# Kernel tuning notes

Measured on AMD Instinct MI355X. Metric: run time of the kernel, lower is better.

## Reference

```python
import jax, jax.numpy as jnp
import numpy as np
from jax import lax

# Module config (matches init_kwargs)
FILTERS = 4
C, D_K, H, W = 4, 3, 128, 128   # kernel_size = [c, d, h, w]
ACT_SIZE = (3, 3, 3)            # activate_size
ACT_STRIDE = (3, 1, 1)          # activate_stride
LEAKY_ALPHA = 0.2               # tf.nn.leaky_relu default
BATCH, DEPTH = 4, 16


def setup_inputs() -> dict:
    key = jax.random.key(0)
    kx, kw, kb = jax.random.split(key, 3)
    x = jax.random.normal(kx, (BATCH, C, DEPTH, H, W), jnp.float32)
    # he_normal on the [filters,1,c,d,h,w] maps (fan_in = c*d*h*w)
    scale = np.float32(np.sqrt(2.0 / (C * D_K * H * W)))
    weight = jax.random.normal(kw, (FILTERS, 1, C, D_K, H, W), jnp.float32) * scale
    bias = jax.random.normal(kb, (FILTERS, 1, C, D_K, H, W), jnp.float32) * scale
    return {"x": x, "weight": weight, "bias": bias}


def _forward(x, weight, bias):
    # x: [B, c, D, h, w]; weight/bias: [F, 1, c, d, h, w]
    B, c, D, h, w = x.shape
    F, d = weight.shape[0], weight.shape[3]
    Dout = D - d + 1  # valid depth windows (try/except skips the out-of-range tails)

    # Sliding depth windows: [B, c, Dout, d, h, w] -> [B, Dout, c, d, h, w]
    idx = jnp.arange(Dout)[:, None] + jnp.arange(d)[None, :]
    xw = jnp.transpose(x[:, :, idx], (0, 2, 1, 3, 4, 5))

    # Per-filter affine on each window (vectorized over F and Dout):
    # a[b,f,i] = x_window[b,i] * weight[f,0] + bias[f,0]  -> [B, F, Dout, c, d, h, w]
    a = xw[:, None] * weight[:, 0][None, :, None] + bias[:, 0][None, :, None]
    a = a.reshape(B * F * Dout, c, d, h, w)

    # Non-trainable 'activate' conv: Conv3D(filters=1, kernel=ones, SAME,
    # channels_first, no bias) followed by leaky_relu(alpha=0.2)
    kern = jnp.ones((1, c) + ACT_SIZE, a.dtype)  # OIDHW
    y = lax.conv_general_dilated(
        a, kern, window_strides=ACT_STRIDE, padding='SAME',
        dimension_numbers=('NCDHW', 'OIDHW', 'NCDHW'))
    y = jax.nn.leaky_relu(y, LEAKY_ALPHA)  # [B*F*Dout, 1, dout, h, w]

    dout = y.shape[2]  # = 1 for d=3, stride 3 (SAME)
    # Concatenation over filters (axis=1) then depth (axis=2)
    return y.reshape(B, F, Dout * dout, h, w)


def reference(x, weight, bias):
    return _forward(x, weight, bias)
```

## Files before the change

### kernel.cpp

```cpp
#include <hip/hip_runtime.h>

#define HH    128
#define WW    128
#define CDIM  4
#define DK    3
#define FDIM  4
#define DEPTH 16
#define DOUT  14
#define NB    4
#define HW    (HH * WW)
#define IB    2
#define NIP   (DOUT / IB)
#define TROWS 4
#define HROWS (TROWS + 2)
#define NTILE (HH / TROWS)

__global__ __launch_bounds__(256) void bsum_kernel(const float* __restrict__ bias,
                                                   float* __restrict__ bsum) {
    int idx = blockIdx.x * 256 + threadIdx.x;
    int f  = idx >> 14;
    int hw = idx & 16383;
    const float* bp = bias + f * (CDIM * DK * HW) + hw;
    float s = 0.f;
#pragma unroll
    for (int c = 0; c < CDIM; ++c)
#pragma unroll
        for (int dd = 0; dd < DK; ++dd)
            s += bp[c * (DK * HW) + dd * HW];
    bsum[idx] = s;
}

__global__ __launch_bounds__(256) void linerconv_main(const float* __restrict__ x,
                                                      const float* __restrict__ wgt,
                                                      const float* __restrict__ bsum,
                                                      float* __restrict__ out) {
    const int blk  = blockIdx.x;
    const int tile = blk & (NTILE - 1);
    const int tmp  = blk >> 5;
    const int ip   = tmp % NIP;
    const int b    = tmp / NIP;
    const int i0   = ip * IB;
    const int h0   = tile * TROWS;

    __shared__ float lds[IB][FDIM][HROWS][WW];

    const int tid = threadIdx.x;

    if (tid < HROWS * 32) {
        const int row = tid >> 5;
        const int q   = tid & 31;
        const int g   = h0 - 1 + row;
        if (g >= 0 && g < HH) {
            const int base_hw = g * WW + q * 4;
            float4 a0[FDIM], a1[FDIM];
#pragma unroll
            for (int f = 0; f < FDIM; ++f) {
                float4 bv = *(const float4*)(bsum + f * HW + base_hw);
                a0[f] = bv;
                a1[f] = bv;
            }
            const float* xb = x + b * (CDIM * DEPTH * HW) + i0 * HW + base_hw;
            const float* wb = wgt + base_hw;
#pragma unroll
            for (int c = 0; c < CDIM; ++c) {
                float4 xp[IB + DK - 1];
#pragma unroll
                for (int j = 0; j < IB + DK - 1; ++j)
                    xp[j] = *(const float4*)(xb + c * (DEPTH * HW) + j * HW);
#pragma unroll
                for (int dd = 0; dd < DK; ++dd) {
#pragma unroll
                    for (int f = 0; f < FDIM; ++f) {
                        float4 wv = *(const float4*)(wb + f * (CDIM * DK * HW)
                                                        + c * (DK * HW) + dd * HW);
                        a0[f].x += xp[dd].x * wv.x;
                        a0[f].y += xp[dd].y * wv.y;
                        a0[f].z += xp[dd].z * wv.z;
                        a0[f].w += xp[dd].w * wv.w;
                        a1[f].x += xp[dd + 1].x * wv.x;
                        a1[f].y += xp[dd + 1].y * wv.y;
                        a1[f].z += xp[dd + 1].z * wv.z;
                        a1[f].w += xp[dd + 1].w * wv.w;
                    }
                }
            }
#pragma unroll
            for (int f = 0; f < FDIM; ++f) {
                *(float4*)&lds[0][f][row][q * 4] = a0[f];
                *(float4*)&lds[1][f][row][q * 4] = a1[f];
            }
        } else {
            float4 z = make_float4(0.f, 0.f, 0.f, 0.f);
#pragma unroll
            for (int f = 0; f < FDIM; ++f) {
                *(float4*)&lds[0][f][row][q * 4] = z;
                *(float4*)&lds[1][f][row][q * 4] = z;
            }
        }
    }
    __syncthreads();

    const int w = tid & 127;
    const int s = tid >> 7;
#pragma unroll
    for (int k = 0; k < 4; ++k) {
        const int i2 = k >> 1;
        const int f  = (k & 1) + s * 2;
        const float* Lb = &lds[i2][f][0][0];
        float rs[HROWS];
#pragma unroll
        for (int g = 0; g < HROWS; ++g) {
            const float* Lr = Lb + g * WW;
            float v = Lr[w];
            if (w > 0)   v += Lr[w - 1];
            if (w < 127) v += Lr[w + 1];
            rs[g] = v;
        }
        float* op = out + ((b * FDIM + f) * DOUT + (i0 + i2)) * HW + h0 * WW + w;
#pragma unroll
        for (int r = 0; r < TROWS; ++r) {
            float sum = rs[r] + rs[r + 1] + rs[r + 2];
            float y = (sum >= 0.f) ? sum : 0.2f * sum;
            __builtin_nontemporal_store(y, op + r * WW);
        }
    }
}

extern "C" void kernel_launch(void* const* d_in, const int* in_sizes, int n_in,
                              void* d_out, int out_size, void* d_ws, size_t ws_size,
                              hipStream_t stream) {
    const float* x    = (const float*)d_in[0];
    const float* wgt  = (const float*)d_in[1];
    const float* bias = (const float*)d_in[2];
    float* out  = (float*)d_out;
    float* bsum = (float*)d_ws;

    bsum_kernel<<<256, 256, 0, stream>>>(bias, bsum);
    linerconv_main<<<NB * NIP * NTILE, 256, 0, stream>>>(x, wgt, bsum, out);
}
```

Baseline: 20.89 us.

## Process four depth windows per block and vectorize the box-filter stage

Each block now computes four output depth windows instead of two, with a two-window tail group, so each x slice and weight load is reused across more windows and fewer blocks re-read overlapping inputs. The second stage now has each thread handle four adjacent columns with float4 LDS reads and float4 nontemporal stores, replacing scalar per-column work. Launch bounds add a minimum of two blocks per CU. In exchange, LDS use and register pressure rise, the grid shrinks from 896 to 512 blocks, and the tail blocks do uneven work.

```diff
diff --git a/kernel.cpp b/kernel.cpp
--- a/kernel.cpp
+++ b/kernel.cpp
@@ -9,11 +9,12 @@
 #define DOUT  14
 #define NB    4
 #define HW    (HH * WW)
-#define IB    2
-#define NIP   (DOUT / IB)
 #define TROWS 4
 #define HROWS (TROWS + 2)
 #define NTILE (HH / TROWS)
+#define NIG   4
+
+typedef float nfloat4 __attribute__((ext_vector_type(4)));
 
 __global__ __launch_bounds__(256) void bsum_kernel(const float* __restrict__ bias,
                                                    float* __restrict__ bsum) {
@@ -30,19 +31,19 @@
     bsum[idx] = s;
 }
 
-__global__ __launch_bounds__(256) void linerconv_main(const float* __restrict__ x,
-                                                      const float* __restrict__ wgt,
-                                                      const float* __restrict__ bsum,
-                                                      float* __restrict__ out) {
+__global__ __launch_bounds__(256, 2) void linerconv_main(const float* __restrict__ x,
+                                                         const float* __restrict__ wgt,
+                                                         const float* __restrict__ bsum,
+                                                         float* __restrict__ out) {
     const int blk  = blockIdx.x;
     const int tile = blk & (NTILE - 1);
-    const int tmp  = blk >> 5;
-    const int ip   = tmp % NIP;
-    const int b    = tmp / NIP;
-    const int i0   = ip * IB;
+    const int ig   = (blk >> 5) & (NIG - 1);
+    const int b    = blk >> 7;
+    const int i0   = ig * 4;
     const int h0   = tile * TROWS;
+    const bool full = (ig != NIG - 1);
 
-    __shared__ float lds[IB][FDIM][HROWS][WW];
+    __shared__ float lds[4][FDIM][HROWS][WW];
 
     const int tid = threadIdx.x;
 
@@ -52,78 +53,123 @@
         const int g   = h0 - 1 + row;
         if (g >= 0 && g < HH) {
             const int base_hw = g * WW + q * 4;
-            float4 a0[FDIM], a1[FDIM];
+            const float* xb = x + (b * CDIM * DEPTH + i0) * HW + base_hw;
+            const float* wb = wgt + base_hw;
+            if (full) {
+                float4 acc[4][FDIM];
 #pragma unroll
-            for (int f = 0; f < FDIM; ++f) {
-                float4 bv = *(const float4*)(bsum + f * HW + base_hw);
-                a0[f] = bv;
-                a1[f] = bv;
-            }
-            const float* xb = x + b * (CDIM * DEPTH * HW) + i0 * HW + base_hw;
-            const float* wb = wgt + base_hw;
+                for (int f = 0; f < FDIM; ++f) {
+                    float4 bv = *(const float4*)(bsum + f * HW + base_hw);
 #pragma unroll
-            for (int c = 0; c < CDIM; ++c) {
-                float4 xp[IB + DK - 1];
+                    for (int i2 = 0; i2 < 4; ++i2) acc[i2][f] = bv;
+                }
 #pragma unroll
-                for (int j = 0; j < IB + DK - 1; ++j)
-                    xp[j] = *(const float4*)(xb + c * (DEPTH * HW) + j * HW);
+                for (int c = 0; c < CDIM; ++c) {
+                    float4 xp[6];
 #pragma unroll
-                for (int dd = 0; dd < DK; ++dd) {
+                    for (int j = 0; j < 6; ++j)
+                        xp[j] = *(const float4*)(xb + c * (DEPTH * HW) + j * HW);
 #pragma unroll
-                    for (int f = 0; f < FDIM; ++f) {
-                        float4 wv = *(const float4*)(wb + f * (CDIM * DK * HW)
-                                                        + c * (DK * HW) + dd * HW);
-                        a0[f].x += xp[dd].x * wv.x;
-                        a0[f].y += xp[dd].y * wv.y;
-                        a0[f].z += xp[dd].z * wv.z;
-                        a0[f].w += xp[dd].w * wv.w;
-                        a1[f].x += xp[dd + 1].x * wv.x;
-                        a1[f].y += xp[dd + 1].y * wv.y;
-                        a1[f].z += xp[dd + 1].z * wv.z;
-                        a1[f].w += xp[dd + 1].w * wv.w;
+                    for (int dd = 0; dd < DK; ++dd) {
+#pragma unroll
+                        for (int f = 0; f < FDIM; ++f) {
+                            float4 wv = *(const float4*)(wb + ((f * CDIM + c) * DK + dd) * HW);
+#pragma unroll
+                            for (int i2 = 0; i2 < 4; ++i2) {
+                                acc[i2][f].x += xp[i2 + dd].x * wv.x;
+                                acc[i2][f].y += xp[i2 + dd].y * wv.y;
+                                acc[i2][f].z += xp[i2 + dd].z * wv.z;
+                                acc[i2][f].w += xp[i2 + dd].w * wv.w;
+                            }
+                        }
                     }
                 }
-            }
 #pragma unroll
-            for (int f = 0; f < FDIM; ++f) {
-                *(float4*)&lds[0][f][row][q * 4] = a0[f];
-                *(float4*)&lds[1][f][row][q * 4] = a1[f];
+                for (int i2 = 0; i2 < 4; ++i2)
+#pragma unroll
+                    for (int f = 0; f < FDIM; ++f)
+                        *(float4*)&lds[i2][f][row][q * 4] = acc[i2][f];
+            } else {
+                float4 acc[2][FDIM];
+#pragma unroll
+                for (int f = 0; f < FDIM; ++f) {
+                    float4 bv = *(const float4*)(bsum + f * HW + base_hw);
+                    acc[0][f] = bv;
+                    acc[1][f] = bv;
+                }
+#pragma unroll
+                for (int c = 0; c < CDIM; ++c) {
+                    float4 xp[4];
+#pragma unroll
+                    for (int j = 0; j < 4; ++j)
+                        xp[j] = *(const float4*)(xb + c * (DEPTH * HW) + j * HW);
+#pragma unroll
+                    for (int dd = 0; dd < DK; ++dd) {
+#pragma unroll
+                        for (int f = 0; f < FDIM; ++f) {
+                            float4 wv = *(const float4*)(wb + ((f * CDIM + c) * DK + dd) * HW);
+#pragma unroll
+                            for (int i2 = 0; i2 < 2; ++i2) {
+                                acc[i2][f].x += xp[i2 + dd].x * wv.x;
+                                acc[i2][f].y += xp[i2 + dd].y * wv.y;
+                                acc[i2][f].z += xp[i2 + dd].z * wv.z;
+                                acc[i2][f].w += xp[i2 + dd].w * wv.w;
+                            }
+                        }
+                    }
+                }
+#pragma unroll
+                for (int i2 = 0; i2 < 2; ++i2)
+#pragma unroll
+                    for (int f = 0; f < FDIM; ++f)
+                        *(float4*)&lds[i2][f][row][q * 4] = acc[i2][f];
             }
         } else {
             float4 z = make_float4(0.f, 0.f, 0.f, 0.f);
 #pragma unroll
-            for (int f = 0; f < FDIM; ++f) {
-                *(float4*)&lds[0][f][row][q * 4] = z;
-                *(float4*)&lds[1][f][row][q * 4] = z;
-            }
+            for (int i2 = 0; i2 < 4; ++i2)
+#pragma unroll
+                for (int f = 0; f < FDIM; ++f)
+                    *(float4*)&lds[i2][f][row][q * 4] = z;
         }
     }
     __syncthreads();
 
-    const int w = tid & 127;
-    const int s = tid >> 7;
-#pragma unroll
-    for (int k = 0; k < 4; ++k) {
-        const int i2 = k >> 1;
-        const int f  = (k & 1) + s * 2;
+    auto do_quadcol = [&](int idx) {
+        const int q  = idx & 31;
+        const int f  = (idx >> 5) & 3;
+        const int i2 = idx >> 7;
         const float* Lb = &lds[i2][f][0][0];
-        float rs[HROWS];
+        float4 rs[HROWS];
 #pragma unroll
         for (int g = 0; g < HROWS; ++g) {
             const float* Lr = Lb + g * WW;
-            float v = Lr[w];
-            if (w > 0)   v += Lr[w - 1];
-            if (w < 127) v += Lr[w + 1];
-            rs[g] = v;
+            float4 m  = *(const float4*)(Lr + q * 4);
+            float lft = (q > 0)  ? Lr[q * 4 - 1] : 0.f;
+            float rgt = (q < 31) ? Lr[q * 4 + 4] : 0.f;
+            rs[g].x = lft + m.x + m.y;
+            rs[g].y = m.x + m.y + m.z;
+            rs[g].z = m.y + m.z + m.w;
+            rs[g].w = m.z + m.w + rgt;
         }
-        float* op = out + ((b * FDIM + f) * DOUT + (i0 + i2)) * HW + h0 * WW + w;
+        float* op = out + ((b * FDIM + f) * DOUT + (i0 + i2)) * HW + h0 * WW + q * 4;
 #pragma unroll
         for (int r = 0; r < TROWS; ++r) {
-            float sum = rs[r] + rs[r + 1] + rs[r + 2];
-            float y = (sum >= 0.f) ? sum : 0.2f * sum;
-            __builtin_nontemporal_store(y, op + r * WW);
+            nfloat4 s;
+            s.x = rs[r].x + rs[r + 1].x + rs[r + 2].x;
+            s.y = rs[r].y + rs[r + 1].y + rs[r + 2].y;
+            s.z = rs[r].z + rs[r + 1].z + rs[r + 2].z;
+            s.w = rs[r].w + rs[r + 1].w + rs[r + 2].w;
+            s.x = (s.x >= 0.f) ? s.x : 0.2f * s.x;
+            s.y = (s.y >= 0.f) ? s.y : 0.2f * s.y;
+            s.z = (s.z >= 0.f) ? s.z : 0.2f * s.z;
+            s.w = (s.w >= 0.f) ? s.w : 0.2f * s.w;
+            __builtin_nontemporal_store(s, (nfloat4*)(op + r * WW));
         }
-    }
+    };
+    do_quadcol(tid);
+    if (full) do_quadcol(tid + 256);
+
 }
 
 extern "C" void kernel_launch(void* const* d_in, const int* in_sizes, int n_in,
@@ -136,5 +182,5 @@
     float* bsum = (float*)d_ws;
 
     bsum_kernel<<<256, 256, 0, stream>>>(bias, bsum);
-    linerconv_main<<<NB * NIP * NTILE, 256, 0, stream>>>(x, wgt, bsum, out);
+    linerconv_main<<<NB * NIG * NTILE, 256, 0, stream>>>(x, wgt, bsum, out);
 }
```

Result: faster. 18.50 us (-11.4%).
